# Performance work log

Measured on AMD Instinct MI355X. Metric: run time of the kernel, lower is better.

The kernel has to match this reference:

```python
import jax, jax.numpy as jnp
import numpy as np

EPS = 1e-7
MAX_NORM = 1.0 - 1e-5
N_NODES, K_DEG, D_IN, D_HID, D_OUT, B = 65536, 16, 512, 256, 64, 64


def _norm(x):
    return jnp.sqrt(jnp.sum(x * x, axis=-1, keepdims=True))


def mobius_add(x, y):
    # Poincare ball (c=1) Mobius addition along feature dim
    x2 = jnp.sum(x * x, -1, keepdims=True)
    y2 = jnp.sum(y * y, -1, keepdims=True)
    xy = jnp.sum(x * y, -1, keepdims=True)
    num = (1.0 + 2.0 * xy + y2) * x + (1.0 - x2) * y
    den = 1.0 + 2.0 * xy + x2 * y2
    return num / jnp.maximum(den, EPS)


def mobius_matvec(x, M):
    # geoopt mobius_matvec(W, x) == x @ W.T; here M already oriented (d_in, d_out)
    mx = x @ M
    xn = jnp.clip(_norm(x), EPS, MAX_NORM)
    mxn = jnp.maximum(_norm(mx), EPS)
    return jnp.tanh(mxn / xn * jnp.arctanh(xn)) * mx / mxn


def logmap0(y):
    yn = jnp.clip(_norm(y), EPS, MAX_NORM)
    return jnp.arctanh(yn) * y / yn


def expmap0(v):
    vn = jnp.maximum(_norm(v), EPS)
    return jnp.tanh(vn) * v / vn


def aggregate(feat, src_idx):
    # sequential left-fold mobius_add over each node's K in-neighbor messages
    init = feat[src_idx[:, 0]]  # [N, D]
    def step(acc, idx_k):
        return mobius_add(acc, feat[idx_k]), None
    acc, _ = jax.lax.scan(step, init, src_idx[:, 1:].T)
    return acc


def hyper_conv(feat, src_idx, W, b, in_gt_out):
    K = src_idx.shape[1]
    norm = K ** -0.5  # in-degree is exactly K for every node
    feat = feat * norm
    if in_gt_out:
        feat = mobius_matvec(feat, W)
        rst = aggregate(feat, src_idx)
    else:
        rst = aggregate(feat, src_idx)
        rst = mobius_matvec(rst, W)
    rst = rst * norm
    rst = mobius_add(rst, b)
    # activation: logmap0 -> relu -> expmap0
    return expmap0(jax.nn.relu(logmap0(rst)))


def setup_inputs() -> dict:
    key = jax.random.key(0)
    ks = jax.random.split(key, 8)
    features = 0.02 * jax.random.uniform(ks[0], (N_NODES, D_IN), minval=-1.0, maxval=1.0, dtype=jnp.float32)
    src_idx = jax.random.randint(ks[1], (N_NODES, K_DEG), 0, N_NODES, dtype=jnp.int32)
    to_fetch = jax.random.randint(ks[2], (B,), 0, N_NODES // B, dtype=jnp.int32)
    W1 = 0.051 * jax.random.normal(ks[3], (D_IN, D_HID), dtype=jnp.float32)   # xavier-ish
    b1 = jnp.zeros((D_HID,), dtype=jnp.float32)
    W2 = 0.062 * jax.random.normal(ks[4], (D_HID, D_HID), dtype=jnp.float32)
    b2 = jnp.zeros((D_HID,), dtype=jnp.float32)
    Wl = 0.088 * jax.random.normal(ks[5], (D_OUT, D_HID), dtype=jnp.float32)  # (out, in) like torch Linear
    bl = jnp.zeros((D_OUT,), dtype=jnp.float32)
    return {"features": features, "W1": W1, "b1": b1, "W2": W2, "b2": b2,
            "Wl": Wl, "bl": bl, "src_idx": src_idx, "to_fetch": to_fetch}


def reference(features, W1, b1, W2, b2, Wl, bl, src_idx, to_fetch):
    h = hyper_conv(features, src_idx, W1, b1, True)    # 512 -> 256 (in > out branch)
    h = hyper_conv(h, src_idx, W2, b2, False)          # 256 -> 256 (aggregate first)
    n_per = features.shape[0] // to_fetch.shape[0]     # batched graphs, equal size
    idx = to_fetch + jnp.arange(to_fetch.shape[0], dtype=to_fetch.dtype) * n_per
    h = h[idx]                                         # [B, D_HID]
    h = mobius_add(mobius_matvec(h, Wl.T), bl)         # mobius Linear 256 -> 64
    return h
```

## Files before the change

kernel.cpp:

```cpp
#include <hip/hip_runtime.h>
#include <math.h>

#define EPSF 1e-7f
#define MAXNF (1.0f - 1e-5f)

typedef __attribute__((ext_vector_type(8))) short short8;
typedef __attribute__((ext_vector_type(4))) float f32x4;

union Pun8 { unsigned short u[8]; short8 s; };

static __device__ __forceinline__ unsigned short f2bf_rn(float f) {
  union { float f; unsigned u; } v;
  v.f = f;
  unsigned r = v.u + 0x7fff + ((v.u >> 16) & 1);
  return (unsigned short)(r >> 16);
}
static __device__ __forceinline__ float bf2f(unsigned short h) {
  union { unsigned u; float f; } v;
  v.u = ((unsigned)h) << 16;
  return v.f;
}

template <int CTRL>
static __device__ __forceinline__ float dpp_add(float v) {
  int s = __builtin_amdgcn_update_dpp(0, __float_as_int(v), CTRL, 0xf, 0xf,
                                      true);
  return v + __int_as_float(s);
}
static __device__ __forceinline__ float wsum(float v) {
  v = dpp_add<0x111>(v);
  v = dpp_add<0x112>(v);
  v = dpp_add<0x114>(v);
  v = dpp_add<0x118>(v);
  v = dpp_add<0x142>(v);
  v = dpp_add<0x143>(v);
  return __int_as_float(__builtin_amdgcn_readlane(__float_as_int(v), 63));
}
static __device__ __forceinline__ float hsum16_t(float v) {
  v = dpp_add<0x111>(v);
  v = dpp_add<0x112>(v);
  v = dpp_add<0x114>(v);
  v = dpp_add<0x118>(v);
  return v;
}

__device__ __forceinline__ float dot4(const float4 a, const float4 b) {
  return a.x * b.x + a.y * b.y + a.z * b.z + a.w * b.w;
}
__device__ __forceinline__ float4 mobius_step(const float4 x, const float4 y) {
  float px = wsum(dot4(x, x));
  float py = wsum(dot4(y, y));
  float pxy = wsum(dot4(x, y));
  float cx = 1.f + 2.f * pxy + py;
  float cy = 1.f - px;
  float inv = 1.f / fmaxf(1.f + 2.f * pxy + px * py, EPSF);
  float4 r;
  r.x = (cx * x.x + cy * y.x) * inv;
  r.y = (cx * x.y + cy * y.y) * inv;
  r.z = (cx * x.z + cy * y.z) * inv;
  r.w = (cx * x.w + cy * y.w) * inv;
  return r;
}

__global__ __launch_bounds__(256) void
k0_pack(const float* __restrict__ W1, unsigned short* __restrict__ hi,
        unsigned short* __restrict__ lo) {
  const int id = blockIdx.x * 256 + threadIdx.x;
  const int s = id >> 10;
  const int t = (id >> 6) & 15;
  const int l = id & 63;
  const int n = t * 16 + (l & 15);
  const int k0 = s * 32 + ((l >> 4) << 3);
  Pun8 ph, pl;
#pragma unroll
  for (int jj = 0; jj < 8; ++jj) {
    float wv = W1[(k0 + jj) * 256 + n];
    unsigned short hb = f2bf_rn(wv);
    ph.u[jj] = hb;
    pl.u[jj] = f2bf_rn(wv - bf2f(hb));
  }
  *reinterpret_cast<short8*>(hi + id * 8) = ph.s;
  *reinterpret_cast<short8*>(lo + id * 8) = pl.s;
}

__global__ __launch_bounds__(512, 1) void
k1_h1(const float* __restrict__ features, const unsigned short* __restrict__ bhi,
      const unsigned short* __restrict__ blo, const float* __restrict__ b1,
      const int* __restrict__ src_idx, const int* __restrict__ to_fetch,
      float* __restrict__ h1) {
  const int b4 = blockIdx.x << 2;
  const int tid = threadIdx.x;
  const int w = tid >> 6;
  const int lane = tid & 63;
  const int g = lane >> 4;
  const int r16 = lane & 15;

  __shared__ __align__(16) unsigned short aH[64 * 512];
  __shared__ __align__(16) unsigned short aL[64 * 512];
  __shared__ float s_msp[8][64];
  __shared__ float s_fs2[64], s_srow[64];
  __shared__ int s_anode[4];
  __shared__ int s_vn[64];

  if (tid < 4) {
    const int pair = b4 + tid;
    const int jj = pair >> 4, kk = pair & 15;
    s_anode[tid] = src_idx[(to_fetch[jj] + (jj << 10)) * 16 + kk];
  }
  __syncthreads();
  if (tid < 64) s_vn[tid] = src_idx[s_anode[tid >> 4] * 16 + (tid & 15)];
  __syncthreads();

#pragma unroll
  for (int batch = 0; batch < 2; ++batch) {
    float4 f0[4], f1[4];
    const int rb = (w << 3) + (batch << 2);
#pragma unroll
    for (int i = 0; i < 4; ++i) {
      const float* rp = features + (size_t)s_vn[rb + i] * 512 + lane * 8;
      f0[i] = *reinterpret_cast<const float4*>(rp);
      f1[i] = *reinterpret_cast<const float4*>(rp + 4);
    }
#pragma unroll
    for (int i = 0; i < 4; ++i) {
      const int r = rb + i;
      const float fv[8] = {f0[i].x, f0[i].y, f0[i].z, f0[i].w,
                           f1[i].x, f1[i].y, f1[i].z, f1[i].w};
      Pun8 ph, pl;
      float ss = 0.f;
#pragma unroll
      for (int q = 0; q < 8; ++q) {
        ss = fmaf(fv[q], fv[q], ss);
        unsigned short hb = f2bf_rn(fv[q]);
        ph.u[q] = hb;
        pl.u[q] = f2bf_rn(fv[q] - bf2f(hb));
      }
      const int off = r * 512 + ((lane * 8) ^ ((r & 7) * 8));
      *reinterpret_cast<short8*>(&aH[off]) = ph.s;
      *reinterpret_cast<short8*>(&aL[off]) = pl.s;
      ss = wsum(ss);
      if (lane == 0) s_fs2[r] = ss;
    }
  }
  __syncthreads();

  const int g8 = g * 8;
  const int sw = (r16 & 7) * 8;
  const int tbase = w * 2;
  const short8* Bh = reinterpret_cast<const short8*>(bhi);
  const short8* Bl = reinterpret_cast<const short8*>(blo);

  f32x4 acc[4][2];
#pragma unroll
  for (int p = 0; p < 4; ++p)
#pragma unroll
    for (int i = 0; i < 2; ++i) acc[p][i] = (f32x4){0.f, 0.f, 0.f, 0.f};

  short8 A0[4][2], A1[4][2];
  short8 B0[2][2], B1[2][2];

#define LOADA(AR, S)                                                          \
  {                                                                           \
    const int s_ = (S)&15;                                                    \
    _Pragma("unroll") for (int p_ = 0; p_ < 4; ++p_) {                        \
      const int o_ = ((p_ << 4) + r16) * 512 + (((s_ << 5) + g8) ^ sw);       \
      AR[p_][0] = *reinterpret_cast<const short8*>(&aH[o_]);                  \
      AR[p_][1] = *reinterpret_cast<const short8*>(&aL[o_]);                  \
    }                                                                         \
  }
#define LOADB(BR, S)                                                          \
  {                                                                           \
    const int s_ = (S)&15;                                                    \
    _Pragma("unroll") for (int i_ = 0; i_ < 2; ++i_) {                        \
      const int idx_ = ((s_ << 4) + tbase + i_) * 64 + lane;                  \
      BR[i_][0] = Bh[idx_];                                                   \
      BR[i_][1] = Bl[idx_];                                                   \
    }                                                                         \
  }
#define MFMAALL(AR, BR)                                                       \
  _Pragma("unroll") for (int p_ = 0; p_ < 4; ++p_)                            \
      _Pragma("unroll") for (int i_ = 0; i_ < 2; ++i_) acc[p_][i_] =          \
      __builtin_amdgcn_mfma_f32_16x16x32_bf16(AR[p_][0], BR[i_][0],           \
                                              acc[p_][i_], 0, 0, 0);          \
  _Pragma("unroll") for (int p_ = 0; p_ < 4; ++p_)                            \
      _Pragma("unroll") for (int i_ = 0; i_ < 2; ++i_) acc[p_][i_] =          \
      __builtin_amdgcn_mfma_f32_16x16x32_bf16(AR[p_][0], BR[i_][1],           \
                                              acc[p_][i_], 0, 0, 0);          \
  _Pragma("unroll") for (int p_ = 0; p_ < 4; ++p_)                            \
      _Pragma("unroll") for (int i_ = 0; i_ < 2; ++i_) acc[p_][i_] =          \
      __builtin_amdgcn_mfma_f32_16x16x32_bf16(AR[p_][1], BR[i_][0],           \
                                              acc[p_][i_], 0, 0, 0);

  LOADA(A0, 0)
  LOADB(B0, 0)
#pragma unroll 1
  for (int s = 0; s < 16; s += 2) {
    LOADB(B1, s + 1)
    LOADA(A1, s + 1)
    MFMAALL(A0, B0)
    LOADB(B0, s + 2)
    LOADA(A0, s + 2)
    MFMAALL(A1, B1)
  }

#pragma unroll
  for (int p = 0; p < 4; ++p) {
    float rs[4];
#pragma unroll
    for (int reg = 0; reg < 4; ++reg) {
      float v = fmaf(acc[p][0][reg], acc[p][0][reg],
                     acc[p][1][reg] * acc[p][1][reg]);
      rs[reg] = hsum16_t(v);
    }
    if (r16 == 15) {
#pragma unroll
      for (int reg = 0; reg < 4; ++reg)
        s_msp[w][(p << 4) + (g << 2) + reg] = rs[reg];
    }
  }
  __syncthreads();
  if (tid < 64) {
    float ms2 = 0.f;
#pragma unroll
    for (int ww = 0; ww < 8; ++ww) ms2 += s_msp[ww][tid];
    const float xn = fminf(fmaxf(0.25f * sqrtf(s_fs2[tid]), EPSF), MAXNF);
    const float mxn = fmaxf(0.25f * sqrtf(ms2), EPSF);
    s_srow[tid] = tanhf(mxn / xn * atanhf(xn)) * 0.25f / mxn;
  }
  __syncthreads();

  float(*trow)[256] = reinterpret_cast<float(*)[256]>(&aH[0]);
#pragma unroll
  for (int p = 0; p < 4; ++p) {
#pragma unroll
    for (int i = 0; i < 2; ++i) {
      const int n = ((tbase + i) << 4) + r16;
#pragma unroll
      for (int reg = 0; reg < 4; ++reg) {
        const int row = (p << 4) + (g << 2) + reg;
        trow[row][n] = acc[p][i][reg] * s_srow[row];
      }
    }
  }
  __syncthreads();

  if (w < 4) {
    const int l4 = lane << 2;
    float4 x = *reinterpret_cast<const float4*>(&trow[w * 16][l4]);
#pragma unroll 1
    for (int kk = 1; kk < 16; ++kk) {
      const float4 y = *reinterpret_cast<const float4*>(&trow[w * 16 + kk][l4]);
      x = mobius_step(x, y);
    }
    x.x *= 0.25f; x.y *= 0.25f; x.z *= 0.25f; x.w *= 0.25f;
    {
      const float4 b = *reinterpret_cast<const float4*>(b1 + l4);
      x = mobius_step(x, b);
    }
    float pn = wsum(dot4(x, x));
    float yn = fminf(fmaxf(sqrtf(pn), EPSF), MAXNF);
    float s = atanhf(yn) / yn;
    float4 v;
    v.x = fmaxf(s * x.x, 0.f);
    v.y = fmaxf(s * x.y, 0.f);
    v.z = fmaxf(s * x.z, 0.f);
    v.w = fmaxf(s * x.w, 0.f);
    float pv = wsum(dot4(v, v));
    float vn = fmaxf(sqrtf(pv), EPSF);
    float s2 = tanhf(vn) / vn;
    float4 h;
    h.x = s2 * v.x;
    h.y = s2 * v.y;
    h.z = s2 * v.z;
    h.w = s2 * v.w;
    *reinterpret_cast<float4*>(h1 + (size_t)(b4 + w) * 256 + l4) = h;
  }
#undef LOADA
#undef LOADB
#undef MFMAALL
}

__global__ __launch_bounds__(256) void
k2_out(const float* __restrict__ h1, const float* __restrict__ W2,
       const float* __restrict__ b2, const float* __restrict__ Wl,
       const float* __restrict__ bl, float* __restrict__ out) {
  const int j = blockIdx.x;
  const int tid = threadIdx.x;
  const int w = tid >> 6;
  const int lane = tid & 63;
  const int l4 = lane << 2;

  __shared__ float hrows[16][256];
  __shared__ float xs[256];
  __shared__ float pp[4][256];

  const float* base = h1 + (size_t)j * 4096;
#pragma unroll
  for (int t = 0; t < 4; ++t) {
    const int idx = (t << 8) + tid;
    const int r = idx >> 6;
    const int c4 = (idx & 63) << 2;
    float4 f = *reinterpret_cast<const float4*>(base + r * 256 + c4);
    f.x *= 0.25f; f.y *= 0.25f; f.z *= 0.25f; f.w *= 0.25f;
    *reinterpret_cast<float4*>(&hrows[r][c4]) = f;
  }
  __syncthreads();

  float4 x = make_float4(0.f, 0.f, 0.f, 0.f);
  if (w == 0) {
    x = *reinterpret_cast<const float4*>(&hrows[0][l4]);
#pragma unroll 1
    for (int kk = 1; kk < 16; ++kk) {
      const float4 y = *reinterpret_cast<const float4*>(&hrows[kk][l4]);
      x = mobius_step(x, y);
    }
    *reinterpret_cast<float4*>(&xs[l4]) = x;
  }
  __syncthreads();

  {
    float4 p = make_float4(0.f, 0.f, 0.f, 0.f);
    const int dbase = w << 6;
    for (int d = 0; d < 64; ++d) {
      const float xd = xs[dbase + d];
      const float4 wv =
          *reinterpret_cast<const float4*>(W2 + (size_t)(dbase + d) * 256 + l4);
      p.x = fmaf(xd, wv.x, p.x);
      p.y = fmaf(xd, wv.y, p.y);
      p.z = fmaf(xd, wv.z, p.z);
      p.w = fmaf(xd, wv.w, p.w);
    }
    *reinterpret_cast<float4*>(&pp[w][l4]) = p;
  }
  __syncthreads();

  if (w == 0) {
    float4 mx;
    mx.x = pp[0][l4 + 0] + pp[1][l4 + 0] + pp[2][l4 + 0] + pp[3][l4 + 0];
    mx.y = pp[0][l4 + 1] + pp[1][l4 + 1] + pp[2][l4 + 1] + pp[3][l4 + 1];
    mx.z = pp[0][l4 + 2] + pp[1][l4 + 2] + pp[2][l4 + 2] + pp[3][l4 + 2];
    mx.w = pp[0][l4 + 3] + pp[1][l4 + 3] + pp[2][l4 + 3] + pp[3][l4 + 3];
    {
      float px = wsum(dot4(x, x));
      float pm = wsum(dot4(mx, mx));
      float xn = fminf(fmaxf(sqrtf(px), EPSF), MAXNF);
      float mxn = fmaxf(sqrtf(pm), EPSF);
      float s = tanhf(mxn / xn * atanhf(xn)) / mxn;
      s *= 0.25f;
      x.x = s * mx.x; x.y = s * mx.y; x.z = s * mx.z; x.w = s * mx.w;
    }
    {
      const float4 b = *reinterpret_cast<const float4*>(b2 + l4);
      x = mobius_step(x, b);
    }
    float pn = wsum(dot4(x, x));
    float yn = fminf(fmaxf(sqrtf(pn), EPSF), MAXNF);
    float s = atanhf(yn) / yn;
    float4 v;
    v.x = fmaxf(s * x.x, 0.f);
    v.y = fmaxf(s * x.y, 0.f);
    v.z = fmaxf(s * x.z, 0.f);
    v.w = fmaxf(s * x.w, 0.f);
    float pv = wsum(dot4(v, v));
    float vn = fmaxf(sqrtf(pv), EPSF);
    float s2 = tanhf(vn) / vn;
    float4 h;
    h.x = s2 * v.x; h.y = s2 * v.y; h.z = s2 * v.z; h.w = s2 * v.w;

    *reinterpret_cast<float4*>(&xs[l4]) = h;
    float m = 0.f;
    for (int d = 0; d < 256; d += 4) {
      const float4 wv =
          *reinterpret_cast<const float4*>(Wl + (size_t)lane * 256 + d);
      m = fmaf(wv.x, xs[d + 0], m);
      m = fmaf(wv.y, xs[d + 1], m);
      m = fmaf(wv.z, xs[d + 2], m);
      m = fmaf(wv.w, xs[d + 3], m);
    }
    float ph = wsum(dot4(h, h));
    float pmm = wsum(m * m);
    float hn = fminf(fmaxf(sqrtf(ph), EPSF), MAXNF);
    float mn = fmaxf(sqrtf(pmm), EPSF);
    float sc = tanhf(mn / hn * atanhf(hn)) / mn;
    float mo = sc * m;
    float bo = bl[lane];
    float pxx = wsum(mo * mo);
    float pbb = wsum(bo * bo);
    float pxb = wsum(mo * bo);
    float cx = 1.f + 2.f * pxb + pbb;
    float cy = 1.f - pxx;
    float inv = 1.f / fmaxf(1.f + 2.f * pxb + pxx * pbb, EPSF);
    out[j * 64 + lane] = (cx * mo + cy * bo) * inv;
  }
}

extern "C" void kernel_launch(void* const* d_in, const int* in_sizes, int n_in,
                              void* d_out, int out_size, void* d_ws,
                              size_t ws_size, hipStream_t stream) {
  const float* features = (const float*)d_in[0];
  const float* W1 = (const float*)d_in[1];
  const float* b1 = (const float*)d_in[2];
  const float* W2 = (const float*)d_in[3];
  const float* b2 = (const float*)d_in[4];
  const float* Wl = (const float*)d_in[5];
  const float* bl = (const float*)d_in[6];
  const int* src_idx = (const int*)d_in[7];
  const int* to_fetch = (const int*)d_in[8];
  float* out = (float*)d_out;

  float* h1 = (float*)d_ws;
  unsigned short* whi = (unsigned short*)((char*)d_ws + (1u << 20));
  unsigned short* wlo = (unsigned short*)((char*)d_ws + (1u << 20) + (1u << 18));

  k0_pack<<<64, 256, 0, stream>>>(W1, whi, wlo);
  k1_h1<<<256, 512, 0, stream>>>(features, whi, wlo, b1, src_idx, to_fetch, h1);
  k2_out<<<64, 256, 0, stream>>>(h1, W2, b2, Wl, bl, out);
}
```

Before: 45.91 us.

## Fuse weight packing, gather-GEMM and output stage into one cooperative kernel

Merges the three kernels (W1 bf16 hi/lo packing, first-layer gather+MFMA, second-layer aggregate/output) into a single cooperative launch. Grid-wide syncs separate the phases, and the final stage reuses the GEMM's shared memory on the first 64 blocks. The goal is to remove two kernel launch gaps and inter-kernel idle time. In exchange it adds two grid barriers, has only 64 of 256 blocks working in the last phase, and requires all 256 blocks of 512 threads with large LDS to be co-resident.

```diff
diff --git a/kernel.cpp b/kernel.cpp
--- a/kernel.cpp
+++ b/kernel.cpp
@@ -1,5 +1,8 @@
 #include <hip/hip_runtime.h>
+#include <hip/hip_cooperative_groups.h>
 #include <math.h>
+
+namespace cg = cooperative_groups;
 
 #define EPSF 1e-7f
 #define MAXNF (1.0f - 1e-5f)
@@ -62,32 +65,14 @@
   return r;
 }
 
-__global__ __launch_bounds__(256) void
-k0_pack(const float* __restrict__ W1, unsigned short* __restrict__ hi,
-        unsigned short* __restrict__ lo) {
-  const int id = blockIdx.x * 256 + threadIdx.x;
-  const int s = id >> 10;
-  const int t = (id >> 6) & 15;
-  const int l = id & 63;
-  const int n = t * 16 + (l & 15);
-  const int k0 = s * 32 + ((l >> 4) << 3);
-  Pun8 ph, pl;
-#pragma unroll
-  for (int jj = 0; jj < 8; ++jj) {
-    float wv = W1[(k0 + jj) * 256 + n];
-    unsigned short hb = f2bf_rn(wv);
-    ph.u[jj] = hb;
-    pl.u[jj] = f2bf_rn(wv - bf2f(hb));
-  }
-  *reinterpret_cast<short8*>(hi + id * 8) = ph.s;
-  *reinterpret_cast<short8*>(lo + id * 8) = pl.s;
-}
-
-__global__ __launch_bounds__(512, 1) void
-k1_h1(const float* __restrict__ features, const unsigned short* __restrict__ bhi,
-      const unsigned short* __restrict__ blo, const float* __restrict__ b1,
-      const int* __restrict__ src_idx, const int* __restrict__ to_fetch,
-      float* __restrict__ h1) {
+__global__ __launch_bounds__(512, 2) void
+fused_all(const float* __restrict__ features, const float* __restrict__ W1,
+          unsigned short* __restrict__ whi, unsigned short* __restrict__ wlo,
+          const float* __restrict__ b1, const int* __restrict__ src_idx,
+          const int* __restrict__ to_fetch, float* __restrict__ h1,
+          const float* __restrict__ W2, const float* __restrict__ b2,
+          const float* __restrict__ Wl, const float* __restrict__ bl,
+          float* __restrict__ out) {
   const int b4 = blockIdx.x << 2;
   const int tid = threadIdx.x;
   const int w = tid >> 6;
@@ -102,6 +87,18 @@
   __shared__ int s_anode[4];
   __shared__ int s_vn[64];
 
+  {
+    const int e = (blockIdx.x << 9) | tid;
+    const int id = e >> 3, jj = e & 7;
+    const int s = id >> 10, t = (id >> 6) & 15, l = id & 63;
+    const int n = t * 16 + (l & 15);
+    const int kr = s * 32 + ((l >> 4) << 3) + jj;
+    const float wv = W1[kr * 256 + n];
+    const unsigned short hb = f2bf_rn(wv);
+    whi[id * 8 + jj] = hb;
+    wlo[id * 8 + jj] = f2bf_rn(wv - bf2f(hb));
+  }
+
   if (tid < 4) {
     const int pair = b4 + tid;
     const int jj = pair >> 4, kk = pair & 15;
@@ -144,11 +141,13 @@
   }
   __syncthreads();
 
+  cg::this_grid().sync();
+
   const int g8 = g * 8;
   const int sw = (r16 & 7) * 8;
   const int tbase = w * 2;
-  const short8* Bh = reinterpret_cast<const short8*>(bhi);
-  const short8* Bl = reinterpret_cast<const short8*>(blo);
+  const short8* Bh = reinterpret_cast<const short8*>(whi);
+  const short8* Bl = reinterpret_cast<const short8*>(wlo);
 
   f32x4 acc[4][2];
 #pragma unroll
@@ -278,119 +277,121 @@
 #undef LOADA
 #undef LOADB
 #undef MFMAALL
-}
-
-__global__ __launch_bounds__(256) void
-k2_out(const float* __restrict__ h1, const float* __restrict__ W2,
-       const float* __restrict__ b2, const float* __restrict__ Wl,
-       const float* __restrict__ bl, float* __restrict__ out) {
-  const int j = blockIdx.x;
-  const int tid = threadIdx.x;
-  const int w = tid >> 6;
-  const int lane = tid & 63;
-  const int l4 = lane << 2;
-
-  __shared__ float hrows[16][256];
-  __shared__ float xs[256];
-  __shared__ float pp[4][256];
-
-  const float* base = h1 + (size_t)j * 4096;
-#pragma unroll
-  for (int t = 0; t < 4; ++t) {
-    const int idx = (t << 8) + tid;
-    const int r = idx >> 6;
-    const int c4 = (idx & 63) << 2;
-    float4 f = *reinterpret_cast<const float4*>(base + r * 256 + c4);
-    f.x *= 0.25f; f.y *= 0.25f; f.z *= 0.25f; f.w *= 0.25f;
-    *reinterpret_cast<float4*>(&hrows[r][c4]) = f;
-  }
-  __syncthreads();
-
-  float4 x = make_float4(0.f, 0.f, 0.f, 0.f);
-  if (w == 0) {
-    x = *reinterpret_cast<const float4*>(&hrows[0][l4]);
+
+  cg::this_grid().sync();
+
+  if (blockIdx.x < 64) {
+    const int j = blockIdx.x;
+    const int l4 = lane << 2;
+    float(*hrows)[256] = reinterpret_cast<float(*)[256]>(&aH[0]);
+    float* xs = reinterpret_cast<float*>(&aH[0]) + 16 * 256;
+    float(*pp)[256] =
+        reinterpret_cast<float(*)[256]>(reinterpret_cast<float*>(&aH[0]) +
+                                        16 * 256 + 256);
+
+    __syncthreads();
+
+    const float* base = h1 + (size_t)j * 4096;
+#pragma unroll
+    for (int t = 0; t < 2; ++t) {
+      const int idx = (t << 9) + tid;
+      const int r = idx >> 6;
+      const int c4 = (idx & 63) << 2;
+      float4 f = *reinterpret_cast<const float4*>(base + r * 256 + c4);
+      f.x *= 0.25f; f.y *= 0.25f; f.z *= 0.25f; f.w *= 0.25f;
+      *reinterpret_cast<float4*>(&hrows[r][c4]) = f;
+    }
+    __syncthreads();
+
+    float4 x = make_float4(0.f, 0.f, 0.f, 0.f);
+    if (tid < 64) {
+      x = *reinterpret_cast<const float4*>(&hrows[0][l4]);
 #pragma unroll 1
-    for (int kk = 1; kk < 16; ++kk) {
-      const float4 y = *reinterpret_cast<const float4*>(&hrows[kk][l4]);
-      x = mobius_step(x, y);
-    }
-    *reinterpret_cast<float4*>(&xs[l4]) = x;
-  }
-  __syncthreads();
-
-  {
-    float4 p = make_float4(0.f, 0.f, 0.f, 0.f);
-    const int dbase = w << 6;
-    for (int d = 0; d < 64; ++d) {
-      const float xd = xs[dbase + d];
-      const float4 wv =
-          *reinterpret_cast<const float4*>(W2 + (size_t)(dbase + d) * 256 + l4);
-      p.x = fmaf(xd, wv.x, p.x);
-      p.y = fmaf(xd, wv.y, p.y);
-      p.z = fmaf(xd, wv.z, p.z);
-      p.w = fmaf(xd, wv.w, p.w);
-    }
-    *reinterpret_cast<float4*>(&pp[w][l4]) = p;
-  }
-  __syncthreads();
-
-  if (w == 0) {
-    float4 mx;
-    mx.x = pp[0][l4 + 0] + pp[1][l4 + 0] + pp[2][l4 + 0] + pp[3][l4 + 0];
-    mx.y = pp[0][l4 + 1] + pp[1][l4 + 1] + pp[2][l4 + 1] + pp[3][l4 + 1];
-    mx.z = pp[0][l4 + 2] + pp[1][l4 + 2] + pp[2][l4 + 2] + pp[3][l4 + 2];
-    mx.w = pp[0][l4 + 3] + pp[1][l4 + 3] + pp[2][l4 + 3] + pp[3][l4 + 3];
+      for (int kk = 1; kk < 16; ++kk) {
+        const float4 y = *reinterpret_cast<const float4*>(&hrows[kk][l4]);
+        x = mobius_step(x, y);
+      }
+      *reinterpret_cast<float4*>(&xs[l4]) = x;
+    }
+    __syncthreads();
+
     {
-      float px = wsum(dot4(x, x));
-      float pm = wsum(dot4(mx, mx));
-      float xn = fminf(fmaxf(sqrtf(px), EPSF), MAXNF);
-      float mxn = fmaxf(sqrtf(pm), EPSF);
-      float s = tanhf(mxn / xn * atanhf(xn)) / mxn;
-      s *= 0.25f;
-      x.x = s * mx.x; x.y = s * mx.y; x.z = s * mx.z; x.w = s * mx.w;
-    }
-    {
-      const float4 b = *reinterpret_cast<const float4*>(b2 + l4);
-      x = mobius_step(x, b);
-    }
-    float pn = wsum(dot4(x, x));
-    float yn = fminf(fmaxf(sqrtf(pn), EPSF), MAXNF);
-    float s = atanhf(yn) / yn;
-    float4 v;
-    v.x = fmaxf(s * x.x, 0.f);
-    v.y = fmaxf(s * x.y, 0.f);
-    v.z = fmaxf(s * x.z, 0.f);
-    v.w = fmaxf(s * x.w, 0.f);
-    float pv = wsum(dot4(v, v));
-    float vn = fmaxf(sqrtf(pv), EPSF);
-    float s2 = tanhf(vn) / vn;
-    float4 h;
-    h.x = s2 * v.x; h.y = s2 * v.y; h.z = s2 * v.z; h.w = s2 * v.w;
-
-    *reinterpret_cast<float4*>(&xs[l4]) = h;
-    float m = 0.f;
-    for (int d = 0; d < 256; d += 4) {
-      const float4 wv =
-          *reinterpret_cast<const float4*>(Wl + (size_t)lane * 256 + d);
-      m = fmaf(wv.x, xs[d + 0], m);
-      m = fmaf(wv.y, xs[d + 1], m);
-      m = fmaf(wv.z, xs[d + 2], m);
-      m = fmaf(wv.w, xs[d + 3], m);
-    }
-    float ph = wsum(dot4(h, h));
-    float pmm = wsum(m * m);
-    float hn = fminf(fmaxf(sqrtf(ph), EPSF), MAXNF);
-    float mn = fmaxf(sqrtf(pmm), EPSF);
-    float sc = tanhf(mn / hn * atanhf(hn)) / mn;
-    float mo = sc * m;
-    float bo = bl[lane];
-    float pxx = wsum(mo * mo);
-    float pbb = wsum(bo * bo);
-    float pxb = wsum(mo * bo);
-    float cx = 1.f + 2.f * pxb + pbb;
-    float cy = 1.f - pxx;
-    float inv = 1.f / fmaxf(1.f + 2.f * pxb + pxx * pbb, EPSF);
-    out[j * 64 + lane] = (cx * mo + cy * bo) * inv;
+      float4 p = make_float4(0.f, 0.f, 0.f, 0.f);
+      const int dbase = w << 5;
+      for (int d = 0; d < 32; ++d) {
+        const float xd = xs[dbase + d];
+        const float4 wv = *reinterpret_cast<const float4*>(
+            W2 + (size_t)(dbase + d) * 256 + l4);
+        p.x = fmaf(xd, wv.x, p.x);
+        p.y = fmaf(xd, wv.y, p.y);
+        p.z = fmaf(xd, wv.z, p.z);
+        p.w = fmaf(xd, wv.w, p.w);
+      }
+      *reinterpret_cast<float4*>(&pp[w][l4]) = p;
+    }
+    __syncthreads();
+
+    if (tid < 64) {
+      float4 mx = make_float4(0.f, 0.f, 0.f, 0.f);
+#pragma unroll
+      for (int ww = 0; ww < 8; ++ww) {
+        mx.x += pp[ww][l4 + 0];
+        mx.y += pp[ww][l4 + 1];
+        mx.z += pp[ww][l4 + 2];
+        mx.w += pp[ww][l4 + 3];
+      }
+      {
+        float px = wsum(dot4(x, x));
+        float pm = wsum(dot4(mx, mx));
+        float xn = fminf(fmaxf(sqrtf(px), EPSF), MAXNF);
+        float mxn = fmaxf(sqrtf(pm), EPSF);
+        float s = tanhf(mxn / xn * atanhf(xn)) / mxn;
+        s *= 0.25f;
+        x.x = s * mx.x; x.y = s * mx.y; x.z = s * mx.z; x.w = s * mx.w;
+      }
+      {
+        const float4 b = *reinterpret_cast<const float4*>(b2 + l4);
+        x = mobius_step(x, b);
+      }
+      float pn = wsum(dot4(x, x));
+      float yn = fminf(fmaxf(sqrtf(pn), EPSF), MAXNF);
+      float s = atanhf(yn) / yn;
+      float4 v;
+      v.x = fmaxf(s * x.x, 0.f);
+      v.y = fmaxf(s * x.y, 0.f);
+      v.z = fmaxf(s * x.z, 0.f);
+      v.w = fmaxf(s * x.w, 0.f);
+      float pv = wsum(dot4(v, v));
+      float vn = fmaxf(sqrtf(pv), EPSF);
+      float s2 = tanhf(vn) / vn;
+      float4 h;
+      h.x = s2 * v.x; h.y = s2 * v.y; h.z = s2 * v.z; h.w = s2 * v.w;
+
+      *reinterpret_cast<float4*>(&xs[l4]) = h;
+      float m = 0.f;
+      for (int d = 0; d < 256; d += 4) {
+        const float4 wv =
+            *reinterpret_cast<const float4*>(Wl + (size_t)lane * 256 + d);
+        m = fmaf(wv.x, xs[d + 0], m);
+        m = fmaf(wv.y, xs[d + 1], m);
+        m = fmaf(wv.z, xs[d + 2], m);
+        m = fmaf(wv.w, xs[d + 3], m);
+      }
+      float ph = wsum(dot4(h, h));
+      float pmm = wsum(m * m);
+      float hn = fminf(fmaxf(sqrtf(ph), EPSF), MAXNF);
+      float mn = fmaxf(sqrtf(pmm), EPSF);
+      float sc = tanhf(mn / hn * atanhf(hn)) / mn;
+      float mo = sc * m;
+      float bo = bl[lane];
+      float pxx = wsum(mo * mo);
+      float pbb = wsum(bo * bo);
+      float pxb = wsum(mo * bo);
+      float cx = 1.f + 2.f * pxb + pbb;
+      float cy = 1.f - pxx;
+      float inv = 1.f / fmaxf(1.f + 2.f * pxb + pxx * pbb, EPSF);
+      out[j * 64 + lane] = (cx * mo + cy * bo) * inv;
+    }
   }
 }
 
@@ -412,7 +413,10 @@
   unsigned short* whi = (unsigned short*)((char*)d_ws + (1u << 20));
   unsigned short* wlo = (unsigned short*)((char*)d_ws + (1u << 20) + (1u << 18));
 
-  k0_pack<<<64, 256, 0, stream>>>(W1, whi, wlo);
-  k1_h1<<<256, 512, 0, stream>>>(features, whi, wlo, b1, src_idx, to_fetch, h1);
-  k2_out<<<64, 256, 0, stream>>>(h1, W2, b2, Wl, bl, out);
-}
+  void* args[] = {(void*)&features, (void*)&W1,  (void*)&whi, (void*)&wlo,
+                  (void*)&b1,       (void*)&src_idx, (void*)&to_fetch,
+                  (void*)&h1,       (void*)&W2,  (void*)&b2,  (void*)&Wl,
+                  (void*)&bl,       (void*)&out};
+  hipLaunchCooperativeKernel((void*)fused_all, dim3(256), dim3(512), args, 0,
+                             stream);
+}
```

New measurement: 107.5 us. 2.34x slower.

## Fuse output stage into h1 kernel via last-block atomic counter

Applied to the files above, without the earlier changes.

Removes the separate k2_out launch. Each group of four k1 blocks bumps a per-output atomic counter, and the last block to finish does the aggregation, the W2 matvec split across 8 waves, the activation and the final linear layer, reusing its shared memory. k0_pack zeroes the counters. This drops one kernel launch and the gap between kernels, but adds threadfences, an atomic, and serial tail work on the last block of each group.

```diff
diff --git a/kernel.cpp b/kernel.cpp
--- a/kernel.cpp
+++ b/kernel.cpp
@@ -64,7 +64,8 @@
 
 __global__ __launch_bounds__(256) void
 k0_pack(const float* __restrict__ W1, unsigned short* __restrict__ hi,
-        unsigned short* __restrict__ lo) {
+        unsigned short* __restrict__ lo, int* __restrict__ ctr) {
+  if (blockIdx.x == 0 && threadIdx.x < 64) ctr[threadIdx.x] = 0;
   const int id = blockIdx.x * 256 + threadIdx.x;
   const int s = id >> 10;
   const int t = (id >> 6) & 15;
@@ -84,10 +85,14 @@
 }
 
 __global__ __launch_bounds__(512, 1) void
-k1_h1(const float* __restrict__ features, const unsigned short* __restrict__ bhi,
-      const unsigned short* __restrict__ blo, const float* __restrict__ b1,
-      const int* __restrict__ src_idx, const int* __restrict__ to_fetch,
-      float* __restrict__ h1) {
+k1_fused(const float* __restrict__ features,
+         const unsigned short* __restrict__ bhi,
+         const unsigned short* __restrict__ blo, const float* __restrict__ b1,
+         const int* __restrict__ src_idx, const int* __restrict__ to_fetch,
+         float* __restrict__ h1, const float* __restrict__ W2,
+         const float* __restrict__ b2, const float* __restrict__ Wl,
+         const float* __restrict__ bl, float* __restrict__ out,
+         int* __restrict__ ctr) {
   const int b4 = blockIdx.x << 2;
   const int tid = threadIdx.x;
   const int w = tid >> 6;
@@ -101,6 +106,7 @@
   __shared__ float s_fs2[64], s_srow[64];
   __shared__ int s_anode[4];
   __shared__ int s_vn[64];
+  __shared__ int s_last;
 
   if (tid < 4) {
     const int pair = b4 + tid;
@@ -278,119 +284,123 @@
 #undef LOADA
 #undef LOADB
 #undef MFMAALL
-}
-
-__global__ __launch_bounds__(256) void
-k2_out(const float* __restrict__ h1, const float* __restrict__ W2,
-       const float* __restrict__ b2, const float* __restrict__ Wl,
-       const float* __restrict__ bl, float* __restrict__ out) {
-  const int j = blockIdx.x;
-  const int tid = threadIdx.x;
-  const int w = tid >> 6;
-  const int lane = tid & 63;
-  const int l4 = lane << 2;
-
-  __shared__ float hrows[16][256];
-  __shared__ float xs[256];
-  __shared__ float pp[4][256];
-
-  const float* base = h1 + (size_t)j * 4096;
-#pragma unroll
-  for (int t = 0; t < 4; ++t) {
-    const int idx = (t << 8) + tid;
-    const int r = idx >> 6;
-    const int c4 = (idx & 63) << 2;
-    float4 f = *reinterpret_cast<const float4*>(base + r * 256 + c4);
-    f.x *= 0.25f; f.y *= 0.25f; f.z *= 0.25f; f.w *= 0.25f;
-    *reinterpret_cast<float4*>(&hrows[r][c4]) = f;
-  }
-  __syncthreads();
-
-  float4 x = make_float4(0.f, 0.f, 0.f, 0.f);
-  if (w == 0) {
-    x = *reinterpret_cast<const float4*>(&hrows[0][l4]);
+
+  const int j = blockIdx.x >> 2;
+  __threadfence();
+  __syncthreads();
+  if (tid == 0) s_last = (atomicAdd(&ctr[j], 1) == 3) ? 1 : 0;
+  __syncthreads();
+  if (!s_last) return;
+
+  __threadfence();
+  {
+    const int l4 = lane << 2;
+    float(*hrows)[256] = reinterpret_cast<float(*)[256]>(&aH[0]);
+    float* xs = reinterpret_cast<float*>(&aH[0]) + 16 * 256;
+    float(*pp)[256] = reinterpret_cast<float(*)[256]>(
+        reinterpret_cast<float*>(&aH[0]) + 16 * 256 + 256);
+
+    const float* base = h1 + (size_t)j * 4096;
+#pragma unroll
+    for (int t = 0; t < 2; ++t) {
+      const int idx = (t << 9) + tid;
+      const int r = idx >> 6;
+      const int c4 = (idx & 63) << 2;
+      float4 f = *reinterpret_cast<const float4*>(base + r * 256 + c4);
+      f.x *= 0.25f; f.y *= 0.25f; f.z *= 0.25f; f.w *= 0.25f;
+      *reinterpret_cast<float4*>(&hrows[r][c4]) = f;
+    }
+    __syncthreads();
+
+    float4 x = make_float4(0.f, 0.f, 0.f, 0.f);
+    if (tid < 64) {
+      x = *reinterpret_cast<const float4*>(&hrows[0][l4]);
 #pragma unroll 1
-    for (int kk = 1; kk < 16; ++kk) {
-      const float4 y = *reinterpret_cast<const float4*>(&hrows[kk][l4]);
-      x = mobius_step(x, y);
-    }
-    *reinterpret_cast<float4*>(&xs[l4]) = x;
-  }
-  __syncthreads();
-
-  {
-    float4 p = make_float4(0.f, 0.f, 0.f, 0.f);
-    const int dbase = w << 6;
-    for (int d = 0; d < 64; ++d) {
-      const float xd = xs[dbase + d];
-      const float4 wv =
-          *reinterpret_cast<const float4*>(W2 + (size_t)(dbase + d) * 256 + l4);
-      p.x = fmaf(xd, wv.x, p.x);
-      p.y = fmaf(xd, wv.y, p.y);
-      p.z = fmaf(xd, wv.z, p.z);
-      p.w = fmaf(xd, wv.w, p.w);
-    }
-    *reinterpret_cast<float4*>(&pp[w][l4]) = p;
-  }
-  __syncthreads();
-
-  if (w == 0) {
-    float4 mx;
-    mx.x = pp[0][l4 + 0] + pp[1][l4 + 0] + pp[2][l4 + 0] + pp[3][l4 + 0];
-    mx.y = pp[0][l4 + 1] + pp[1][l4 + 1] + pp[2][l4 + 1] + pp[3][l4 + 1];
-    mx.z = pp[0][l4 + 2] + pp[1][l4 + 2] + pp[2][l4 + 2] + pp[3][l4 + 2];
-    mx.w = pp[0][l4 + 3] + pp[1][l4 + 3] + pp[2][l4 + 3] + pp[3][l4 + 3];
+      for (int kk = 1; kk < 16; ++kk) {
+        const float4 y = *reinterpret_cast<const float4*>(&hrows[kk][l4]);
+        x = mobius_step(x, y);
+      }
+      *reinterpret_cast<float4*>(&xs[l4]) = x;
+    }
+    __syncthreads();
+
     {
-      float px = wsum(dot4(x, x));
-      float pm = wsum(dot4(mx, mx));
-      float xn = fminf(fmaxf(sqrtf(px), EPSF), MAXNF);
-      float mxn = fmaxf(sqrtf(pm), EPSF);
-      float s = tanhf(mxn / xn * atanhf(xn)) / mxn;
-      s *= 0.25f;
-      x.x = s * mx.x; x.y = s * mx.y; x.z = s * mx.z; x.w = s * mx.w;
-    }
-    {
-      const float4 b = *reinterpret_cast<const float4*>(b2 + l4);
-      x = mobius_step(x, b);
-    }
-    float pn = wsum(dot4(x, x));
-    float yn = fminf(fmaxf(sqrtf(pn), EPSF), MAXNF);
-    float s = atanhf(yn) / yn;
-    float4 v;
-    v.x = fmaxf(s * x.x, 0.f);
-    v.y = fmaxf(s * x.y, 0.f);
-    v.z = fmaxf(s * x.z, 0.f);
-    v.w = fmaxf(s * x.w, 0.f);
-    float pv = wsum(dot4(v, v));
-    float vn = fmaxf(sqrtf(pv), EPSF);
-    float s2 = tanhf(vn) / vn;
-    float4 h;
-    h.x = s2 * v.x; h.y = s2 * v.y; h.z = s2 * v.z; h.w = s2 * v.w;
-
-    *reinterpret_cast<float4*>(&xs[l4]) = h;
-    float m = 0.f;
-    for (int d = 0; d < 256; d += 4) {
-      const float4 wv =
-          *reinterpret_cast<const float4*>(Wl + (size_t)lane * 256 + d);
-      m = fmaf(wv.x, xs[d + 0], m);
-      m = fmaf(wv.y, xs[d + 1], m);
-      m = fmaf(wv.z, xs[d + 2], m);
-      m = fmaf(wv.w, xs[d + 3], m);
-    }
-    float ph = wsum(dot4(h, h));
-    float pmm = wsum(m * m);
-    float hn = fminf(fmaxf(sqrtf(ph), EPSF), MAXNF);
-    float mn = fmaxf(sqrtf(pmm), EPSF);
-    float sc = tanhf(mn / hn * atanhf(hn)) / mn;
-    float mo = sc * m;
-    float bo = bl[lane];
-    float pxx = wsum(mo * mo);
-    float pbb = wsum(bo * bo);
-    float pxb = wsum(mo * bo);
-    float cx = 1.f + 2.f * pxb + pbb;
-    float cy = 1.f - pxx;
-    float inv = 1.f / fmaxf(1.f + 2.f * pxb + pxx * pbb, EPSF);
-    out[j * 64 + lane] = (cx * mo + cy * bo) * inv;
+      float4 p = make_float4(0.f, 0.f, 0.f, 0.f);
+      const int dbase = w << 5;
+      for (int d = 0; d < 32; ++d) {
+        const float xd = xs[dbase + d];
+        const float4 wv = *reinterpret_cast<const float4*>(
+            W2 + (size_t)(dbase + d) * 256 + l4);
+        p.x = fmaf(xd, wv.x, p.x);
+        p.y = fmaf(xd, wv.y, p.y);
+        p.z = fmaf(xd, wv.z, p.z);
+        p.w = fmaf(xd, wv.w, p.w);
+      }
+      *reinterpret_cast<float4*>(&pp[w][l4]) = p;
+    }
+    __syncthreads();
+
+    if (tid < 64) {
+      float4 mx = make_float4(0.f, 0.f, 0.f, 0.f);
+#pragma unroll
+      for (int ww = 0; ww < 8; ++ww) {
+        mx.x += pp[ww][l4 + 0];
+        mx.y += pp[ww][l4 + 1];
+        mx.z += pp[ww][l4 + 2];
+        mx.w += pp[ww][l4 + 3];
+      }
+      {
+        float px = wsum(dot4(x, x));
+        float pm = wsum(dot4(mx, mx));
+        float xn = fminf(fmaxf(sqrtf(px), EPSF), MAXNF);
+        float mxn = fmaxf(sqrtf(pm), EPSF);
+        float s = tanhf(mxn / xn * atanhf(xn)) / mxn;
+        s *= 0.25f;
+        x.x = s * mx.x; x.y = s * mx.y; x.z = s * mx.z; x.w = s * mx.w;
+      }
+      {
+        const float4 b = *reinterpret_cast<const float4*>(b2 + l4);
+        x = mobius_step(x, b);
+      }
+      float pn = wsum(dot4(x, x));
+      float yn = fminf(fmaxf(sqrtf(pn), EPSF), MAXNF);
+      float s = atanhf(yn) / yn;
+      float4 v;
+      v.x = fmaxf(s * x.x, 0.f);
+      v.y = fmaxf(s * x.y, 0.f);
+      v.z = fmaxf(s * x.z, 0.f);
+      v.w = fmaxf(s * x.w, 0.f);
+      float pv = wsum(dot4(v, v));
+      float vn = fmaxf(sqrtf(pv), EPSF);
+      float s2 = tanhf(vn) / vn;
+      float4 h;
+      h.x = s2 * v.x; h.y = s2 * v.y; h.z = s2 * v.z; h.w = s2 * v.w;
+
+      *reinterpret_cast<float4*>(&xs[l4]) = h;
+      float m = 0.f;
+      for (int d = 0; d < 256; d += 4) {
+        const float4 wv =
+            *reinterpret_cast<const float4*>(Wl + (size_t)lane * 256 + d);
+        m = fmaf(wv.x, xs[d + 0], m);
+        m = fmaf(wv.y, xs[d + 1], m);
+        m = fmaf(wv.z, xs[d + 2], m);
+        m = fmaf(wv.w, xs[d + 3], m);
+      }
+      float ph = wsum(dot4(h, h));
+      float pmm = wsum(m * m);
+      float hn = fminf(fmaxf(sqrtf(ph), EPSF), MAXNF);
+      float mn = fmaxf(sqrtf(pmm), EPSF);
+      float sc = tanhf(mn / hn * atanhf(hn)) / mn;
+      float mo = sc * m;
+      float bo = bl[lane];
+      float pxx = wsum(mo * mo);
+      float pbb = wsum(bo * bo);
+      float pxb = wsum(mo * bo);
+      float cx = 1.f + 2.f * pxb + pbb;
+      float cy = 1.f - pxx;
+      float inv = 1.f / fmaxf(1.f + 2.f * pxb + pxx * pbb, EPSF);
+      out[j * 64 + lane] = (cx * mo + cy * bo) * inv;
+    }
   }
 }
 
@@ -410,9 +420,11 @@
 
   float* h1 = (float*)d_ws;
   unsigned short* whi = (unsigned short*)((char*)d_ws + (1u << 20));
-  unsigned short* wlo = (unsigned short*)((char*)d_ws + (1u << 20) + (1u << 18));
-
-  k0_pack<<<64, 256, 0, stream>>>(W1, whi, wlo);
-  k1_h1<<<256, 512, 0, stream>>>(features, whi, wlo, b1, src_idx, to_fetch, h1);
-  k2_out<<<64, 256, 0, stream>>>(h1, W2, b2, Wl, bl, out);
-}
+  unsigned short* wlo =
+      (unsigned short*)((char*)d_ws + (1u << 20) + (1u << 18));
+  int* ctr = (int*)((char*)d_ws + (1u << 20) + (1u << 19));
+
+  k0_pack<<<64, 256, 0, stream>>>(W1, whi, wlo, ctr);
+  k1_fused<<<256, 512, 0, stream>>>(features, whi, wlo, b1, src_idx, to_fetch,
+                                    h1, W2, b2, Wl, bl, out, ctr);
+}
```

Result: slower. 98.49 us (+114.5%).
